# Performance work log

Measured on AMD Instinct MI355X. Metric: run time of the kernel, lower is better.

Reference implementation:

```python
import jax, jax.numpy as jnp
import numpy as np


def _sig_gram(X, Y, n):
    """Signature-kernel gram matrix via the Goursat PDE recurrence.
    X: (A, M, D), Y: (B, N, D). Returns (A, B) of k(x_a, y_b).
    Recurrence: K[i+1,j+1] = K[i+1,j] + K[i,j+1] + K[i,j]*(inc_ij - 1).
    """
    f = 2 ** n
    # dyadic refinement: increments scaled by 1/2^n, each repeated 2^n times
    dX = jnp.repeat((X[:, 1:] - X[:, :-1]) / f, f, axis=1)  # (A, Mg-1, D)
    dY = jnp.repeat((Y[:, 1:] - Y[:, :-1]) / f, f, axis=1)  # (B, Ng-1, D)
    inc = jnp.einsum('aid,bjd->abij', dX, dY)               # (A, B, Mg-1, Ng-1)
    A, B, _, Ng1 = inc.shape
    ones_col = jnp.ones((A, B, 1), inc.dtype)

    def row_step(K_prev, inc_row):
        # K_prev: row i of the PDE grid, shape (A,B,Ng1+1); inc_row: (A,B,Ng1)
        diag = K_prev[..., :-1] * (inc_row - 1.0)  # K[i,j]*inc - K[i,j]
        up = K_prev[..., 1:]                        # K[i,j+1]

        def col_step(k_left, uv):
            u, d = uv
            k = k_left + u + d
            return k, k

        _, krow = jax.lax.scan(
            col_step,
            jnp.ones((A, B), inc.dtype),
            (jnp.moveaxis(up, -1, 0), jnp.moveaxis(diag, -1, 0)),
        )
        K_new = jnp.concatenate([ones_col, jnp.moveaxis(krow, 0, -1)], axis=-1)
        return K_new, None

    K0 = jnp.ones((A, B, Ng1 + 1), inc.dtype)  # boundary row K[0,:] = 1
    K_last, _ = jax.lax.scan(row_step, K0, jnp.moveaxis(inc, 2, 0))
    return K_last[..., -1]  # K[-1,-1] for every pair


def setup_inputs() -> dict:
    key = jax.random.key(0)
    kx, ky = jax.random.split(key)
    SCALE = 0.05  # keep kernel values in fp32 range (exponential growth)
    X = jax.random.normal(kx, (64, 128, 16), dtype=jnp.float32) * SCALE
    Y = jax.random.normal(ky, (64, 128, 16), dtype=jnp.float32) * SCALE
    return {"X": X, "Y": Y, "n": 0}


def reference(X, Y, n):
    k_xx = _sig_gram(X, X, n)
    k_yy = _sig_gram(Y, Y, n)
    k_xy = _sig_gram(X, Y, n)
    return jnp.mean(k_xx) + jnp.mean(k_yy) - 2.0 * jnp.mean(k_xy)
```

## Files before the change

kernel.cpp:

```cpp
#include <hip/hip_runtime.h>


#define XY_BLOCKS 1024
#define TRI_BLOCKS 544
#define NBT (XY_BLOCKS + 2 * TRI_BLOCKS)
#define DINC_PER 130048

template <int C, int RM, int BM, bool BC>
__device__ __forceinline__ float dpp0(float x) {
    return __builtin_bit_cast(float, __builtin_amdgcn_update_dpp(
        0, __builtin_bit_cast(int, x), C, RM, BM, BC));
}

__device__ __forceinline__ float wave_scan_incl(float v) {
    v += dpp0<0x111, 0xf, 0xf, true>(v);
    v += dpp0<0x112, 0xf, 0xf, true>(v);
    v += dpp0<0x114, 0xf, 0xf, true>(v);
    v += dpp0<0x118, 0xf, 0xf, true>(v);
    v += dpp0<0x142, 0xa, 0xf, false>(v);
    v += dpp0<0x143, 0xc, 0xf, false>(v);
    return v;
}

__device__ __forceinline__ float wave_shr1(float x, float oldv) {
    return __builtin_bit_cast(float, __builtin_amdgcn_update_dpp(
        __builtin_bit_cast(int, oldv), __builtin_bit_cast(int, x),
        0x138, 0xf, 0xf, false));
}

__global__ __launch_bounds__(256) void sig_diff(
    const float* __restrict__ X, const float* __restrict__ Y,
    float* __restrict__ dInc, float* __restrict__ out)
{
    if (blockIdx.x == 0 && threadIdx.x == 0) out[0] = 0.0f;
    int i = blockIdx.x * 256 + threadIdx.x;
    if (i >= 65024) return;
    int which = (i >= 32512) ? 1 : 0;
    int j = i - which * 32512;
    int a = j / 508;
    int rq = j - a * 508;
    const float* S = which ? Y : X;
    const float4* p = (const float4*)(S + a * 2048) + rq;
    float4 v0 = p[0], v1 = p[4];
    float4 d;
    d.x = v1.x - v0.x; d.y = v1.y - v0.y;
    d.z = v1.z - v0.z; d.w = v1.w - v0.w;
    ((float4*)dInc)[i] = d;
}

__global__ __launch_bounds__(256, 8) void sig_pde8(
    const float* __restrict__ dInc, float* __restrict__ out)
{
    __shared__ float4 Xs4[508];
    __shared__ float red[4];
    const int wid  = threadIdx.x >> 6;
    const int lane = threadIdx.x & 63;
    const int BT   = blockIdx.x;

    int g, a, b0;
    if (BT < XY_BLOCKS) {
        g = 2; a = BT >> 4; b0 = (BT & 15) << 2;
    } else {
        int t = BT - XY_BLOCKS; g = 0;
        if (t >= TRI_BLOCKS) { t -= TRI_BLOCKS; g = 1; }
        int aa = 0;
        for (;;) { int nb = (67 - aa) >> 2; if (t < nb) break; t -= nb; ++aa; }
        a = aa; b0 = aa + (t << 2);
    }
    const int b = b0 + wid;

    const float* dA = (g == 1) ? (dInc + DINC_PER) : dInc;
    const float* dB = (g == 0) ? dInc : (dInc + DINC_PER);

    {
        const float4* Ap = (const float4*)(dA + a * 2032);
        const int tid = threadIdx.x;
        Xs4[tid] = Ap[tid];
        if (tid + 256 < 508) Xs4[tid + 256] = Ap[tid + 256];
    }
    __syncthreads();

    float acc = 0.0f;
    if (g == 2 || b <= 63) {
        const float weight = (g == 2) ? (-2.0f / 4096.0f)
                                      : ((a == b ? 1.0f : 2.0f) / 4096.0f);

        float ya[16], yb_[16];
        {
            const float* Qb = dB + b * 2032;
            const int j0 = lane << 1;
            const int j1 = (j0 + 1 < 127) ? j0 + 1 : 126;
            const float4* A4 = (const float4*)(Qb + j0 * 16);
            const float4* B4 = (const float4*)(Qb + j1 * 16);
#pragma unroll
            for (int q = 0; q < 4; ++q) {
                float4 va = A4[q], vb = B4[q];
                ya[4*q+0]=va.x;  ya[4*q+1]=va.y;  ya[4*q+2]=va.z;  ya[4*q+3]=va.w;
                yb_[4*q+0]=vb.x; yb_[4*q+1]=vb.y; yb_[4*q+2]=vb.z; yb_[4*q+3]=vb.w;
            }
        }

        float g_lo = 1.0f, g_hi = 1.0f;
        const bool last = (lane == 63);

#pragma unroll 1
        for (int r = 0; r < 127; ++r) {
            float xr[16];
#pragma unroll
            for (int q = 0; q < 4; ++q) {
                float4 v = Xs4[4*r + q];
                xr[4*q+0]=v.x; xr[4*q+1]=v.y; xr[4*q+2]=v.z; xr[4*q+3]=v.w;
            }
            float s0 = -0.5f, s1 = -0.5f, t0 = -0.5f, t1 = -0.5f;
#pragma unroll
            for (int d = 0; d < 16; d += 2) {
                s0 = fmaf(xr[d], ya[d], s0);    s1 = fmaf(xr[d+1], ya[d+1], s1);
                t0 = fmaf(xr[d], yb_[d], t0);   t1 = fmaf(xr[d+1], yb_[d+1], t1);
            }
            const float i0 = s0 + s1;
            const float i1 = t0 + t1;

            const float gl = wave_shr1(g_hi, 1.0f);
            const float c0 = fmaf(gl, i0, g_lo);
            const float c1 = last ? 0.0f : fmaf(g_lo, i1, g_hi);
            const float S = wave_scan_incl(c0 + c1);
            g_lo = (S - c1) + 1.0f;
            g_hi = S + 1.0f;
        }

        const float kab = __builtin_bit_cast(float,
            __builtin_amdgcn_readlane(__builtin_bit_cast(int, g_lo), 63));
        acc = weight * kab;
    }

    if (lane == 0) red[wid] = acc;
    __syncthreads();
    if (threadIdx.x == 0)
        atomicAdd(out, (red[0] + red[1]) + (red[2] + red[3]));
}

__global__ __launch_bounds__(256) void sig_reduce2(
    const float* __restrict__ v, float* __restrict__ out, int n)
{
    __shared__ float red[256];
    float s = 0.0f;
    for (int i = threadIdx.x; i < n; i += 256) s += v[i];
    red[threadIdx.x] = s;
    __syncthreads();
    for (int st = 128; st > 0; st >>= 1) {
        if (threadIdx.x < st) red[threadIdx.x] += red[threadIdx.x + st];
        __syncthreads();
    }
    if (threadIdx.x == 0) out[0] = red[0];
}

__global__ __launch_bounds__(64) void sig_pde_kernel(
    const float* __restrict__ X, const float* __restrict__ Y,
    float* __restrict__ ws)
{
    __shared__ float Xs[2048];
    const int T = blockIdx.x;
    const int g = T >> 12;
    const int t = T & 4095;
    const int a = t >> 6, b = t & 63;
    const int lane = threadIdx.x;
    if (g < 2 && a > b) { if (lane == 0) ws[T] = 0.0f; return; }
    const float* P = (g == 1) ? Y : X;
    const float* Q = (g == 0) ? X : Y;
    const float weight = (g == 2) ? (-2.0f / 4096.0f)
                                  : ((a == b ? 1.0f : 2.0f) / 4096.0f);
    {
        const float4* Pa = (const float4*)(P + a * 2048);
        float4* Xs4 = (float4*)Xs;
#pragma unroll
        for (int k = 0; k < 8; ++k) Xs4[lane + (k << 6)] = Pa[lane + (k << 6)];
    }
    __syncthreads();
    {
        float tmp[32];
#pragma unroll
        for (int k = 0; k < 32; ++k) {
            int idx = lane + (k << 6);
            tmp[k] = (idx < 2032) ? (Xs[idx + 16] - Xs[idx]) : 0.0f;
        }
        __syncthreads();
#pragma unroll
        for (int k = 0; k < 32; ++k) {
            int idx = lane + (k << 6);
            if (idx < 2032) Xs[idx] = tmp[k];
        }
    }
    __syncthreads();
    float y0[16], y1[16];
    {
        const float* Qb = Q + b * 2048;
        const int r0 = lane << 1;
        const int r2 = (r0 + 2 > 127) ? 127 : (r0 + 2);
        const float4* A4 = (const float4*)(Qb + r0 * 16);
        const float4* B4 = (const float4*)(Qb + (r0 + 1) * 16);
        const float4* C4 = (const float4*)(Qb + r2 * 16);
#pragma unroll
        for (int q = 0; q < 4; ++q) {
            float4 ra = A4[q], rb = B4[q], rc = C4[q];
            y0[4*q+0] = rb.x - ra.x;  y1[4*q+0] = rc.x - rb.x;
            y0[4*q+1] = rb.y - ra.y;  y1[4*q+1] = rc.y - rb.y;
            y0[4*q+2] = rb.z - ra.z;  y1[4*q+2] = rc.z - rb.z;
            y0[4*q+3] = rb.w - ra.w;  y1[4*q+3] = rc.w - rb.w;
        }
    }
    float g_lo = 1.0f, g_hi = 1.0f;
    const bool last = (lane == 63);
    for (int r = 0; r < 127; ++r) {
        const float* xrow = Xs + r * 16;
        float s0 = -0.5f, s1 = -0.5f, t0 = -0.5f, t1 = -0.5f;
#pragma unroll
        for (int d = 0; d < 16; d += 2) {
            s0 = fmaf(xrow[d], y0[d], s0);   s1 = fmaf(xrow[d+1], y0[d+1], s1);
            t0 = fmaf(xrow[d], y1[d], t0);   t1 = fmaf(xrow[d+1], y1[d+1], t1);
        }
        const float i0 = s0 + s1, i1 = t0 + t1;
        const float gl = wave_shr1(g_hi, 1.0f);
        const float c0 = fmaf(gl, i0, g_lo);
        const float c1 = last ? 0.0f : fmaf(g_lo, i1, g_hi);
        const float S = wave_scan_incl(c0 + c1);
        g_lo = (S - c1) + 1.0f;
        g_hi = S + 1.0f;
    }
    const float kab = __builtin_bit_cast(float,
        __builtin_amdgcn_readlane(__builtin_bit_cast(int, g_lo), 63));
    if (lane == 0) ws[T] = weight * kab;
}

extern "C" void kernel_launch(void* const* d_in, const int* in_sizes, int n_in,
                              void* d_out, int out_size, void* d_ws, size_t ws_size,
                              hipStream_t stream) {
    const float* X = (const float*)d_in[0];
    const float* Y = (const float*)d_in[1];
    float* out = (float*)d_out;
    float* ws  = (float*)d_ws;

    const size_t need = (size_t)(2 * DINC_PER) * sizeof(float);
    if (ws_size >= need) {
        sig_diff<<<254, 256, 0, stream>>>(X, Y, ws, out);
        sig_pde8<<<NBT, 256, 0, stream>>>(ws, out);
    } else {
        sig_pde_kernel<<<12288, 64, 0, stream>>>(X, Y, ws);
        sig_reduce2<<<1, 256, 0, stream>>>(ws, out, 12288);
    }
}
```

Measured before the change: 134.5 us.

## Store increments in lane-fragment layout for coalesced loads and unrolled row pairs

The diff kernel now writes path increments in a fragment layout. Even and odd rows are split, components are grouped by float4 quarter, and each quarter is padded to 64 entries, with one extra block zeroing the padding slot. The PDE kernel can then load each lane's two Y increments with coalesced float4 reads. It also unrolls the row loop by two with a macro that works directly on float4 registers. The aim is to cut uncoalesced global loads and register shuffling; the cost is a more complex index layout and an extra block to zero the padding.

```diff
diff --git a/kernel.cpp b/kernel.cpp
--- a/kernel.cpp
+++ b/kernel.cpp
@@ -4,7 +4,7 @@
 #define XY_BLOCKS 1024
 #define TRI_BLOCKS 544
 #define NBT (XY_BLOCKS + 2 * TRI_BLOCKS)
-#define DINC_PER 130048
+#define FRAG_MAT 32768
 
 template <int C, int RM, int BM, bool BC>
 __device__ __forceinline__ float dpp0(float x) {
@@ -32,26 +32,38 @@
     const float* __restrict__ X, const float* __restrict__ Y,
     float* __restrict__ dInc, float* __restrict__ out)
 {
+    float4* F = (float4*)dInc;
+    if (blockIdx.x == 254) {
+        int t = threadIdx.x;
+#pragma unroll
+        for (int s = 0; s < 2; ++s, t += 256) {
+            int mat = t >> 8, rem = t & 255;
+            int path = rem >> 2, q = rem & 3;
+            F[mat * FRAG_MAT + path * 512 + 256 + q * 64 + 63] =
+                make_float4(0.f, 0.f, 0.f, 0.f);
+        }
+        return;
+    }
     if (blockIdx.x == 0 && threadIdx.x == 0) out[0] = 0.0f;
     int i = blockIdx.x * 256 + threadIdx.x;
-    if (i >= 65024) return;
     int which = (i >= 32512) ? 1 : 0;
     int j = i - which * 32512;
     int a = j / 508;
     int rq = j - a * 508;
+    int r = rq >> 2, q = rq & 3;
     const float* S = which ? Y : X;
     const float4* p = (const float4*)(S + a * 2048) + rq;
     float4 v0 = p[0], v1 = p[4];
     float4 d;
     d.x = v1.x - v0.x; d.y = v1.y - v0.y;
     d.z = v1.z - v0.z; d.w = v1.w - v0.w;
-    ((float4*)dInc)[i] = d;
-}
-
-__global__ __launch_bounds__(256, 8) void sig_pde8(
+    F[which * FRAG_MAT + a * 512 + (r & 1) * 256 + q * 64 + (r >> 1)] = d;
+}
+
+__global__ __launch_bounds__(256, 8) void sig_pde9(
     const float* __restrict__ dInc, float* __restrict__ out)
 {
-    __shared__ float4 Xs4[508];
+    __shared__ float4 Xs4[512];
     __shared__ float red[4];
     const int wid  = threadIdx.x >> 6;
     const int lane = threadIdx.x & 63;
@@ -69,14 +81,14 @@
     }
     const int b = b0 + wid;
 
-    const float* dA = (g == 1) ? (dInc + DINC_PER) : dInc;
-    const float* dB = (g == 0) ? dInc : (dInc + DINC_PER);
-
-    {
-        const float4* Ap = (const float4*)(dA + a * 2032);
+    const float4* F  = (const float4*)dInc;
+    const float4* Af = F + ((g == 1) ? FRAG_MAT : 0) + a * 512;
+    const float4* Bf = F + ((g == 0) ? 0 : FRAG_MAT) + b * 512;
+
+    {
         const int tid = threadIdx.x;
-        Xs4[tid] = Ap[tid];
-        if (tid + 256 < 508) Xs4[tid + 256] = Ap[tid + 256];
+        Xs4[tid]       = Af[tid];
+        Xs4[tid + 256] = Af[tid + 256];
     }
     __syncthreads();
 
@@ -85,48 +97,61 @@
         const float weight = (g == 2) ? (-2.0f / 4096.0f)
                                       : ((a == b ? 1.0f : 2.0f) / 4096.0f);
 
-        float ya[16], yb_[16];
-        {
-            const float* Qb = dB + b * 2032;
-            const int j0 = lane << 1;
-            const int j1 = (j0 + 1 < 127) ? j0 + 1 : 126;
-            const float4* A4 = (const float4*)(Qb + j0 * 16);
-            const float4* B4 = (const float4*)(Qb + j1 * 16);
-#pragma unroll
-            for (int q = 0; q < 4; ++q) {
-                float4 va = A4[q], vb = B4[q];
-                ya[4*q+0]=va.x;  ya[4*q+1]=va.y;  ya[4*q+2]=va.z;  ya[4*q+3]=va.w;
-                yb_[4*q+0]=vb.x; yb_[4*q+1]=vb.y; yb_[4*q+2]=vb.z; yb_[4*q+3]=vb.w;
-            }
-        }
+        float4 ya0 = Bf[       lane], ya1 = Bf[ 64 + lane],
+               ya2 = Bf[128 + lane], ya3 = Bf[192 + lane];
+        float4 yb0 = Bf[256 + lane], yb1 = Bf[320 + lane],
+               yb2 = Bf[384 + lane], yb3 = Bf[448 + lane];
 
         float g_lo = 1.0f, g_hi = 1.0f;
         const bool last = (lane == 63);
 
+#define SIG_ROW(x0,x1,x2,x3)                                                \
+        {                                                                   \
+            float s0=-0.5f, s1=-0.5f, t0=-0.5f, t1=-0.5f;                   \
+            s0=fmaf(x0.x,ya0.x,s0); s1=fmaf(x0.y,ya0.y,s1);                 \
+            t0=fmaf(x0.x,yb0.x,t0); t1=fmaf(x0.y,yb0.y,t1);                 \
+            s0=fmaf(x0.z,ya0.z,s0); s1=fmaf(x0.w,ya0.w,s1);                 \
+            t0=fmaf(x0.z,yb0.z,t0); t1=fmaf(x0.w,yb0.w,t1);                 \
+            s0=fmaf(x1.x,ya1.x,s0); s1=fmaf(x1.y,ya1.y,s1);                 \
+            t0=fmaf(x1.x,yb1.x,t0); t1=fmaf(x1.y,yb1.y,t1);                 \
+            s0=fmaf(x1.z,ya1.z,s0); s1=fmaf(x1.w,ya1.w,s1);                 \
+            t0=fmaf(x1.z,yb1.z,t0); t1=fmaf(x1.w,yb1.w,t1);                 \
+            s0=fmaf(x2.x,ya2.x,s0); s1=fmaf(x2.y,ya2.y,s1);                 \
+            t0=fmaf(x2.x,yb2.x,t0); t1=fmaf(x2.y,yb2.y,t1);                 \
+            s0=fmaf(x2.z,ya2.z,s0); s1=fmaf(x2.w,ya2.w,s1);                 \
+            t0=fmaf(x2.z,yb2.z,t0); t1=fmaf(x2.w,yb2.w,t1);                 \
+            s0=fmaf(x3.x,ya3.x,s0); s1=fmaf(x3.y,ya3.y,s1);                 \
+            t0=fmaf(x3.x,yb3.x,t0); t1=fmaf(x3.y,yb3.y,t1);                 \
+            s0=fmaf(x3.z,ya3.z,s0); s1=fmaf(x3.w,ya3.w,s1);                 \
+            t0=fmaf(x3.z,yb3.z,t0); t1=fmaf(x3.w,yb3.w,t1);                 \
+            const float i0 = s0 + s1;                 \
+            const float i1 = t0 + t1;                 \
+            const float gl = wave_shr1(g_hi, 1.0f);           \
+            const float c0 = fmaf(gl, i0, g_lo);                            \
+            const float c1 = last ? 0.0f : fmaf(g_lo, i1, g_hi);            \
+            const float S  = wave_scan_incl(c0 + c1);                       \
+            g_lo = (S - c1) + 1.0f;                                         \
+            g_hi = S + 1.0f;                                                \
+        }
+
 #pragma unroll 1
-        for (int r = 0; r < 127; ++r) {
-            float xr[16];
-#pragma unroll
-            for (int q = 0; q < 4; ++q) {
-                float4 v = Xs4[4*r + q];
-                xr[4*q+0]=v.x; xr[4*q+1]=v.y; xr[4*q+2]=v.z; xr[4*q+3]=v.w;
+        for (int k = 0; k < 63; ++k) {
+            const float4* rp = &Xs4[k];
+            {
+                float4 x0 = rp[0],   x1 = rp[64],  x2 = rp[128], x3 = rp[192];
+                SIG_ROW(x0, x1, x2, x3)
             }
-            float s0 = -0.5f, s1 = -0.5f, t0 = -0.5f, t1 = -0.5f;
-#pragma unroll
-            for (int d = 0; d < 16; d += 2) {
-                s0 = fmaf(xr[d], ya[d], s0);    s1 = fmaf(xr[d+1], ya[d+1], s1);
-                t0 = fmaf(xr[d], yb_[d], t0);   t1 = fmaf(xr[d+1], yb_[d+1], t1);
+            {
+                float4 x0 = rp[256], x1 = rp[320], x2 = rp[384], x3 = rp[448];
+                SIG_ROW(x0, x1, x2, x3)
             }
-            const float i0 = s0 + s1;
-            const float i1 = t0 + t1;
-
-            const float gl = wave_shr1(g_hi, 1.0f);
-            const float c0 = fmaf(gl, i0, g_lo);
-            const float c1 = last ? 0.0f : fmaf(g_lo, i1, g_hi);
-            const float S = wave_scan_incl(c0 + c1);
-            g_lo = (S - c1) + 1.0f;
-            g_hi = S + 1.0f;
-        }
+        }
+        {
+            const float4* rp = &Xs4[63];
+            float4 x0 = rp[0], x1 = rp[64], x2 = rp[128], x3 = rp[192];
+            SIG_ROW(x0, x1, x2, x3)
+        }
+#undef SIG_ROW
 
         const float kab = __builtin_bit_cast(float,
             __builtin_amdgcn_readlane(__builtin_bit_cast(int, g_lo), 63));
@@ -239,10 +264,10 @@
     float* out = (float*)d_out;
     float* ws  = (float*)d_ws;
 
-    const size_t need = (size_t)(2 * DINC_PER) * sizeof(float);
+    const size_t need = (size_t)(2 * FRAG_MAT) * sizeof(float4);
     if (ws_size >= need) {
-        sig_diff<<<254, 256, 0, stream>>>(X, Y, ws, out);
-        sig_pde8<<<NBT, 256, 0, stream>>>(ws, out);
+        sig_diff<<<255, 256, 0, stream>>>(X, Y, ws, out);
+        sig_pde9<<<NBT, 256, 0, stream>>>(ws, out);
     } else {
         sig_pde_kernel<<<12288, 64, 0, stream>>>(X, Y, ws);
         sig_reduce2<<<1, 256, 0, stream>>>(ws, out, 12288);
```

After: 141.6 us. +5.3%, slower.

## Split PDE columns into two 64-wide passes with LDS boundary column handoff

Applied to the files above, without the earlier changes.

Each wave used to handle two PDE columns per lane over 127 rows. Now it makes two passes of one column per lane. The first pass covers columns 0-63 and stores its right boundary column into shared memory. The second pass covers columns 64-126 and reads that boundary as its left edge. This halves per-lane register use and FMAs per step, which should help occupancy and shorten the per-row dependency chain. The cost is twice as many sequential scan steps, since there are two 127-row passes, plus extra LDS traffic.

```diff
diff --git a/kernel.cpp b/kernel.cpp
--- a/kernel.cpp
+++ b/kernel.cpp
@@ -48,10 +48,11 @@
     ((float4*)dInc)[i] = d;
 }
 
-__global__ __launch_bounds__(256, 8) void sig_pde8(
+__global__ __launch_bounds__(256, 8) void sig_pde10(
     const float* __restrict__ dInc, float* __restrict__ out)
 {
     __shared__ float4 Xs4[508];
+    __shared__ float colbuf[4][128];
     __shared__ float red[4];
     const int wid  = threadIdx.x >> 6;
     const int lane = threadIdx.x & 63;
@@ -84,52 +85,75 @@
     if (g == 2 || b <= 63) {
         const float weight = (g == 2) ? (-2.0f / 4096.0f)
                                       : ((a == b ? 1.0f : 2.0f) / 4096.0f);
-
-        float ya[16], yb_[16];
+        const float* Qb = dB + b * 2032;
+        float* cb = colbuf[wid];
+        const bool last = (lane == 63);
+
+
+        float ya[16];
         {
-            const float* Qb = dB + b * 2032;
-            const int j0 = lane << 1;
-            const int j1 = (j0 + 1 < 127) ? j0 + 1 : 126;
-            const float4* A4 = (const float4*)(Qb + j0 * 16);
-            const float4* B4 = (const float4*)(Qb + j1 * 16);
-#pragma unroll
-            for (int q = 0; q < 4; ++q) {
-                float4 va = A4[q], vb = B4[q];
-                ya[4*q+0]=va.x;  ya[4*q+1]=va.y;  ya[4*q+2]=va.z;  ya[4*q+3]=va.w;
-                yb_[4*q+0]=vb.x; yb_[4*q+1]=vb.y; yb_[4*q+2]=vb.z; yb_[4*q+3]=vb.w;
-            }
-        }
-
-        float g_lo = 1.0f, g_hi = 1.0f;
-        const bool last = (lane == 63);
-
-#pragma unroll 1
+            const float4* Y4 = (const float4*)(Qb + lane * 16);
+#pragma unroll
+            for (int q = 0; q < 4; ++q) {
+                float4 v = Y4[q];
+                ya[4*q+0]=v.x; ya[4*q+1]=v.y; ya[4*q+2]=v.z; ya[4*q+3]=v.w;
+            }
+        }
+        if (last) cb[0] = 1.0f;
+        float gc = 1.0f;
+#pragma unroll 2
         for (int r = 0; r < 127; ++r) {
-            float xr[16];
-#pragma unroll
-            for (int q = 0; q < 4; ++q) {
-                float4 v = Xs4[4*r + q];
-                xr[4*q+0]=v.x; xr[4*q+1]=v.y; xr[4*q+2]=v.z; xr[4*q+3]=v.w;
-            }
-            float s0 = -0.5f, s1 = -0.5f, t0 = -0.5f, t1 = -0.5f;
-#pragma unroll
-            for (int d = 0; d < 16; d += 2) {
-                s0 = fmaf(xr[d], ya[d], s0);    s1 = fmaf(xr[d+1], ya[d+1], s1);
-                t0 = fmaf(xr[d], yb_[d], t0);   t1 = fmaf(xr[d+1], yb_[d+1], t1);
+            const float4* rp = &Xs4[4 * r];
+            float s0 = -0.5f, s1 = -0.5f;
+#pragma unroll
+            for (int q = 0; q < 4; ++q) {
+                float4 v = rp[q];
+                s0 = fmaf(v.x, ya[4*q+0], s0);
+                s1 = fmaf(v.y, ya[4*q+1], s1);
+                s0 = fmaf(v.z, ya[4*q+2], s0);
+                s1 = fmaf(v.w, ya[4*q+3], s1);
             }
             const float i0 = s0 + s1;
-            const float i1 = t0 + t1;
-
-            const float gl = wave_shr1(g_hi, 1.0f);
-            const float c0 = fmaf(gl, i0, g_lo);
-            const float c1 = last ? 0.0f : fmaf(g_lo, i1, g_hi);
-            const float S = wave_scan_incl(c0 + c1);
-            g_lo = (S - c1) + 1.0f;
-            g_hi = S + 1.0f;
+            const float gl = wave_shr1(gc, 1.0f);
+            const float d  = fmaf(gl, i0, gc);
+            const float S  = wave_scan_incl(d);
+            gc = S + 1.0f;
+            if (last) cb[r + 1] = gc;
+        }
+
+        {
+            const int jr = (64 + lane < 127) ? 64 + lane : 126;
+            const float4* Y4 = (const float4*)(Qb + jr * 16);
+#pragma unroll
+            for (int q = 0; q < 4; ++q) {
+                float4 v = Y4[q];
+                ya[4*q+0]=v.x; ya[4*q+1]=v.y; ya[4*q+2]=v.z; ya[4*q+3]=v.w;
+            }
+        }
+        gc = 1.0f;
+#pragma unroll 2
+        for (int r = 0; r < 127; ++r) {
+            const float e0 = cb[r];
+            const float e1 = cb[r + 1];
+            const float4* rp = &Xs4[4 * r];
+            float s0 = -0.5f, s1 = -0.5f;
+#pragma unroll
+            for (int q = 0; q < 4; ++q) {
+                float4 v = rp[q];
+                s0 = fmaf(v.x, ya[4*q+0], s0);
+                s1 = fmaf(v.y, ya[4*q+1], s1);
+                s0 = fmaf(v.z, ya[4*q+2], s0);
+                s1 = fmaf(v.w, ya[4*q+3], s1);
+            }
+            const float i0 = s0 + s1;
+            const float gl = wave_shr1(gc, e0);
+            const float d  = fmaf(gl, i0, gc);
+            const float S  = wave_scan_incl(d);
+            gc = S + e1;
         }
 
         const float kab = __builtin_bit_cast(float,
-            __builtin_amdgcn_readlane(__builtin_bit_cast(int, g_lo), 63));
+            __builtin_amdgcn_readlane(__builtin_bit_cast(int, gc), 62));
         acc = weight * kab;
     }
 
@@ -242,7 +266,7 @@
     const size_t need = (size_t)(2 * DINC_PER) * sizeof(float);
     if (ws_size >= need) {
         sig_diff<<<254, 256, 0, stream>>>(X, Y, ws, out);
-        sig_pde8<<<NBT, 256, 0, stream>>>(ws, out);
+        sig_pde10<<<NBT, 256, 0, stream>>>(ws, out);
     } else {
         sig_pde_kernel<<<12288, 64, 0, stream>>>(X, Y, ws);
         sig_reduce2<<<1, 256, 0, stream>>>(ws, out, 12288);
```

After: 158.9 us. +18.2%, slower.
